# Kernel tuning notes

Hardware: AMD Instinct MI355X
Metric: run time of the kernel (lower is better)

Reference implementation:

```python
import jax, jax.numpy as jnp
import numpy as np

B = 2048          # batch size
L = 8192          # number of fine-grained labels
G = 256           # meta_label_size (number of label groups)
BETA = 0.01       # config.beta


def setup_inputs() -> dict:
    key = jax.random.key(0)
    k1, k2, k3 = jax.random.split(key, 3)
    logits = jax.random.normal(k1, (B, L), dtype=jnp.float32)
    true_y = jax.random.randint(k2, (B, L), 0, 2, dtype=jnp.int32)
    group_ids = jax.random.randint(k3, (L,), 0, G, dtype=jnp.int32)
    return {"logits": logits, "true_y": true_y, "group_ids": group_ids}


def reference(logits, true_y, group_ids):
    # y_hat = sigmoid(logits); meta_prob[b, g] = prod_{l in group g} (1 - y_hat[b, l])
    # Using 1 - sigmoid(x) = sigmoid(-x):
    #   log meta_prob = segment_sum(log_sigmoid(-logits)) over labels per group.
    log_not = jax.nn.log_sigmoid(-logits)                                    # [B, L]
    grp_log = jax.ops.segment_sum(log_not.T, group_ids, num_segments=G).T    # [B, G]
    meta_probs = jnp.exp(grp_log)                                            # [B, G]

    # meta_y[b, g] = 1 if any true label of group g is set in row b (generate_meta_y)
    any_true = jax.ops.segment_sum(true_y.T.astype(jnp.float32), group_ids,
                                   num_segments=G).T                         # [B, G]
    meta_y = (any_true > 0).astype(logits.dtype)

    # BCELoss (mean reduction, torch clamps log terms at -100)
    log_p = jnp.maximum(grp_log, -100.0)
    log_1mp = jnp.maximum(jnp.log1p(-meta_probs), -100.0)
    bce = -jnp.mean(meta_y * log_p + (1.0 - meta_y) * log_1mp)
    return bce * BETA
```

## Files before the change

kernel.cpp:

```cpp
#include <hip/hip_runtime.h>
#include <math.h>

constexpr int   B_    = 2048;
constexpr int   L_    = 8192;
constexpr int   G_    = 256;
constexpr float BETA_ = 0.01f;
constexpr float BIG_  = 1024.0f;

constexpr int   HALF  = L_ / 2;
constexpr int   PMAX  = HALF + G_ * 3;

__device__ __forceinline__ float log_sigmoid_neg(float x) {
    return -(fmaxf(x, 0.0f) + __logf(1.0f + __expf(-fabsf(x))));
}

extern "C" __global__ __launch_bounds__(1024)
void build_rank_kernel(const int* __restrict__ group_ids,
                       int* __restrict__ g_offs,
                       unsigned short* __restrict__ g_rank)
{
    __shared__ int s_cnt[G_];
    __shared__ int s_scan[G_];
    __shared__ int s_cur[G_];

    const int t = threadIdx.x;
    const int h = blockIdx.x;

    if (t < G_) s_cnt[t] = 0;

    const int4 ids = ((const int4*)group_ids)[h * 1024 + t];
    __syncthreads();

    atomicAdd(&s_cnt[ids.x], 1);
    atomicAdd(&s_cnt[ids.y], 1);
    atomicAdd(&s_cnt[ids.z], 1);
    atomicAdd(&s_cnt[ids.w], 1);
    __syncthreads();

    if (t < G_) s_scan[t] = (s_cnt[t] + 3) & ~3;
    __syncthreads();
    for (int off = 1; off < G_; off <<= 1) {
        int v = 0;
        if (t < G_ && t >= off) v = s_scan[t - off];
        __syncthreads();
        if (t < G_) s_scan[t] += v;
        __syncthreads();
    }

    if (t < G_) {
        const int excl = s_scan[t] - ((s_cnt[t] + 3) & ~3);
        s_cur[t] = excl;
        g_offs[h * 257 + t] = excl;
    }
    if (t == 0) g_offs[h * 257 + G_] = s_scan[G_ - 1];
    __syncthreads();

    const int l = h * HALF + t * 4;
    g_rank[l + 0] = (unsigned short)atomicAdd(&s_cur[ids.x], 1);
    g_rank[l + 1] = (unsigned short)atomicAdd(&s_cur[ids.y], 1);
    g_rank[l + 2] = (unsigned short)atomicAdd(&s_cur[ids.z], 1);
    g_rank[l + 3] = (unsigned short)atomicAdd(&s_cur[ids.w], 1);
}


extern "C" __global__ __launch_bounds__(256, 8)
void meta_loss_kernel(const float* __restrict__ logits,
                      const int*   __restrict__ true_y,
                      const int*   __restrict__ g_offs,
                      const unsigned short* __restrict__ g_rank,
                      float*       __restrict__ partial)
{
    __shared__ float s_row[PMAX];

    const int t = threadIdx.x;
    const int b = blockIdx.x >> 1;
    const int h = blockIdx.x & 1;

    const float4*  lg = (const float4*)(logits + (size_t)b * L_ + h * HALF);
    const int4*    ty = (const int4*)(true_y + (size_t)b * L_ + h * HALF);
    const ushort4* rk = (const ushort4*)(g_rank + h * HALF);
    float4* s_row4 = (float4*)s_row;

    const int o0 = g_offs[h * 257 + t];
    const int o1 = g_offs[h * 257 + t + 1];

    #pragma unroll
    for (int i = 0; i < 5; ++i) {
        const int j = i * 256 + t;
        if (j < PMAX / 4) s_row4[j] = make_float4(0.f, 0.f, 0.f, 0.f);
    }
    __syncthreads();

    #pragma unroll
    for (int i = 0; i < HALF / (4 * 256); ++i) {
        const int idx = i * 256 + t;
        const float4  x = lg[idx];
        const int4    y = ty[idx];
        const ushort4 r = rk[idx];
        s_row[r.x] = log_sigmoid_neg(x.x) + (y.x ? BIG_ : 0.0f);
        s_row[r.y] = log_sigmoid_neg(x.y) + (y.y ? BIG_ : 0.0f);
        s_row[r.z] = log_sigmoid_neg(x.z) + (y.z ? BIG_ : 0.0f);
        s_row[r.w] = log_sigmoid_neg(x.w) + (y.w ? BIG_ : 0.0f);
    }
    __syncthreads();

    float4 a4 = make_float4(0.f, 0.f, 0.f, 0.f);
    for (int j = o0; j < o1; j += 4) {
        const float4 v = *(const float4*)&s_row[j];
        a4.x += v.x; a4.y += v.y; a4.z += v.z; a4.w += v.w;
    }
    const float enc = (a4.x + a4.y) + (a4.z + a4.w);

    if (o1 > o0)
        atomicAdd(&partial[b * G_ + t], enc);
}

extern "C" __global__ __launch_bounds__(1024)
void finalize_kernel(const float* __restrict__ partial,
                     float* __restrict__ out)
{
    __shared__ float s_part[16];

    const int t   = threadIdx.x;
    const int idx = blockIdx.x * 1024 + t;

    const float enc = partial[idx];
    const int   k   = __float2int_rn(enc * (1.0f / BIG_));
    const float gl  = enc - BIG_ * (float)k;

    float term;
    if (k != 0) {
        term = fmaxf(gl, -100.0f);
    } else {
        term = fmaxf(log1pf(-__expf(gl)), -100.0f);
    }

    #pragma unroll
    for (int off = 32; off > 0; off >>= 1)
        term += __shfl_down(term, off, 64);
    if ((t & 63) == 0) s_part[t >> 6] = term;
    __syncthreads();

    if (t == 0) {
        float s = 0.0f;
        #pragma unroll
        for (int w = 0; w < 16; ++w) s += s_part[w];
        atomicAdd(out, s * (-BETA_ / ((float)B_ * (float)G_)));
    }
}

extern "C" void kernel_launch(void* const* d_in, const int* in_sizes, int n_in,
                              void* d_out, int out_size, void* d_ws, size_t ws_size,
                              hipStream_t stream) {
    const float* logits    = (const float*)d_in[0];
    const int*   true_y    = (const int*)d_in[1];
    const int*   group_ids = (const int*)d_in[2];
    float*       out       = (float*)d_out;

    float*          partial = (float*)d_ws;
    unsigned short* g_rank  = (unsigned short*)((char*)d_ws + (size_t)B_ * G_ * 4);
    int*            g_offs  = (int*)((char*)d_ws + (size_t)B_ * G_ * 4 + L_ * 2);

    hipMemsetAsync(partial, 0, (size_t)B_ * G_ * 4, stream);
    hipMemsetAsync(out, 0, sizeof(float), stream);

    build_rank_kernel<<<2, 1024, 0, stream>>>(group_ids, g_offs, g_rank);
    meta_loss_kernel<<<2 * B_, 256, 0, stream>>>(logits, true_y, g_offs, g_rank, partial);
    finalize_kernel<<<(B_ * G_) / 1024, 1024, 0, stream>>>(partial, out);
}
```

Measured before the change: 45.28 us.

## Replace scatter-into-sorted-row with permutation gather over 16-label segments

The prep kernel now builds a single global permutation of labels sorted by group, padded to 16-label segments with a sentinel index, plus a per-segment group id. The main kernel uses one 1024-thread block per row: it writes the encoded log-sigmoid values to shared memory in a swizzled order, then each thread gathers one 16-element segment through the permutation and atomically adds the sum to that row's group. This removes the zero-fill and the random shared-memory scatter, at the cost of more atomics per row and indexed shared gathers. It also adds an extra probe kernel that reads half of the logits and throws the result away, which looks like a cache-warming or bandwidth experiment and adds memory traffic.

```diff
diff --git a/kernel.cpp b/kernel.cpp
--- a/kernel.cpp
+++ b/kernel.cpp
@@ -7,37 +7,44 @@
 constexpr float BETA_ = 0.01f;
 constexpr float BIG_  = 1024.0f;
 
-constexpr int   HALF  = L_ / 2;
-constexpr int   PMAX  = HALF + G_ * 3;
+constexpr int   SENTW  = 8192;
+constexpr int   ENCW   = 8256;
+constexpr int   PCAP   = 12032;
+constexpr int   SEGCAP = 768;
 
 __device__ __forceinline__ float log_sigmoid_neg(float x) {
     return -(fmaxf(x, 0.0f) + __logf(1.0f + __expf(-fabsf(x))));
 }
 
+__device__ __forceinline__ int swzF(int l) {
+    return (((l >> 2) & 1) << 12) + ((l >> 3) << 2) + (l & 3);
+}
+
 extern "C" __global__ __launch_bounds__(1024)
-void build_rank_kernel(const int* __restrict__ group_ids,
-                       int* __restrict__ g_offs,
-                       unsigned short* __restrict__ g_rank)
+void prep_kernel(const int* __restrict__ group_ids,
+                 unsigned short* __restrict__ perm,
+                 unsigned char*  __restrict__ seg_gid,
+                 int*            __restrict__ hdr)
 {
     __shared__ int s_cnt[G_];
     __shared__ int s_scan[G_];
     __shared__ int s_cur[G_];
 
     const int t = threadIdx.x;
-    const int h = blockIdx.x;
-
     if (t < G_) s_cnt[t] = 0;
 
-    const int4 ids = ((const int4*)group_ids)[h * 1024 + t];
+    const int4 a = ((const int4*)group_ids)[2 * t];
+    const int4 bq = ((const int4*)group_ids)[2 * t + 1];
     __syncthreads();
 
-    atomicAdd(&s_cnt[ids.x], 1);
-    atomicAdd(&s_cnt[ids.y], 1);
-    atomicAdd(&s_cnt[ids.z], 1);
-    atomicAdd(&s_cnt[ids.w], 1);
+    atomicAdd(&s_cnt[a.x], 1);  atomicAdd(&s_cnt[a.y], 1);
+    atomicAdd(&s_cnt[a.z], 1);  atomicAdd(&s_cnt[a.w], 1);
+    atomicAdd(&s_cnt[bq.x], 1); atomicAdd(&s_cnt[bq.y], 1);
+    atomicAdd(&s_cnt[bq.z], 1); atomicAdd(&s_cnt[bq.w], 1);
     __syncthreads();
 
-    if (t < G_) s_scan[t] = (s_cnt[t] + 3) & ~3;
+    int n = 0, pc = 0;
+    if (t < G_) { n = s_cnt[t]; pc = (n + 15) & ~15; s_scan[t] = pc; }
     __syncthreads();
     for (int off = 1; off < G_; off <<= 1) {
         int v = 0;
@@ -48,71 +55,89 @@
     }
 
     if (t < G_) {
-        const int excl = s_scan[t] - ((s_cnt[t] + 3) & ~3);
-        s_cur[t] = excl;
-        g_offs[h * 257 + t] = excl;
+        const int gbase = s_scan[t] - pc;
+        s_cur[t] = gbase;
+        const int segb = gbase >> 4;
+        for (int i = 0; i < (pc >> 4); ++i) seg_gid[segb + i] = (unsigned char)t;
+        for (int i = n; i < pc; ++i)        perm[gbase + i] = (unsigned short)SENTW;
     }
-    if (t == 0) g_offs[h * 257 + G_] = s_scan[G_ - 1];
+    if (t == 0) hdr[0] = s_scan[G_ - 1] >> 4;
     __syncthreads();
 
-    const int l = h * HALF + t * 4;
-    g_rank[l + 0] = (unsigned short)atomicAdd(&s_cur[ids.x], 1);
-    g_rank[l + 1] = (unsigned short)atomicAdd(&s_cur[ids.y], 1);
-    g_rank[l + 2] = (unsigned short)atomicAdd(&s_cur[ids.z], 1);
-    g_rank[l + 3] = (unsigned short)atomicAdd(&s_cur[ids.w], 1);
+    const int l = 8 * t;
+    perm[atomicAdd(&s_cur[a.x], 1)]  = (unsigned short)swzF(l + 0);
+    perm[atomicAdd(&s_cur[a.y], 1)]  = (unsigned short)swzF(l + 1);
+    perm[atomicAdd(&s_cur[a.z], 1)]  = (unsigned short)swzF(l + 2);
+    perm[atomicAdd(&s_cur[a.w], 1)]  = (unsigned short)swzF(l + 3);
+    perm[atomicAdd(&s_cur[bq.x], 1)] = (unsigned short)swzF(l + 4);
+    perm[atomicAdd(&s_cur[bq.y], 1)] = (unsigned short)swzF(l + 5);
+    perm[atomicAdd(&s_cur[bq.z], 1)] = (unsigned short)swzF(l + 6);
+    perm[atomicAdd(&s_cur[bq.w], 1)] = (unsigned short)swzF(l + 7);
 }
 
+extern "C" __global__ __launch_bounds__(256)
+void probe_kernel(const float* __restrict__ src)
+{
+    const float4* p = (const float4*)src;
+    const size_t  i = (size_t)blockIdx.x * 256 + threadIdx.x;
+    float4 s = make_float4(0.f, 0.f, 0.f, 0.f);
+    #pragma unroll
+    for (int k = 0; k < 4; ++k) {
+        const float4 v = p[i + (size_t)k * 524288];
+        s.x += v.x; s.y += v.y; s.z += v.z; s.w += v.w;
+    }
+    asm volatile("" :: "v"(s.x), "v"(s.y), "v"(s.z), "v"(s.w));
+}
 
-extern "C" __global__ __launch_bounds__(256, 8)
-void meta_loss_kernel(const float* __restrict__ logits,
-                      const int*   __restrict__ true_y,
-                      const int*   __restrict__ g_offs,
-                      const unsigned short* __restrict__ g_rank,
-                      float*       __restrict__ partial)
+extern "C" __global__ __launch_bounds__(1024, 8)
+void meta_gather_kernel(const float* __restrict__ logits,
+                        const int*   __restrict__ true_y,
+                        const unsigned short* __restrict__ perm,
+                        const unsigned char*  __restrict__ seg_gid,
+                        const int*   __restrict__ hdr,
+                        float*       __restrict__ partial)
 {
-    __shared__ float s_row[PMAX];
+    __shared__ float s_enc[ENCW];
 
     const int t = threadIdx.x;
-    const int b = blockIdx.x >> 1;
-    const int h = blockIdx.x & 1;
+    const int b = blockIdx.x;
 
-    const float4*  lg = (const float4*)(logits + (size_t)b * L_ + h * HALF);
-    const int4*    ty = (const int4*)(true_y + (size_t)b * L_ + h * HALF);
-    const ushort4* rk = (const ushort4*)(g_rank + h * HALF);
-    float4* s_row4 = (float4*)s_row;
+    if (t == 0) s_enc[SENTW] = 0.0f;
 
-    const int o0 = g_offs[h * 257 + t];
-    const int o1 = g_offs[h * 257 + t + 1];
+    const float4* lg4 = (const float4*)(logits + (size_t)b * L_);
+    const int4*   ty4 = (const int4*)(true_y + (size_t)b * L_);
 
-    #pragma unroll
-    for (int i = 0; i < 5; ++i) {
-        const int j = i * 256 + t;
-        if (j < PMAX / 4) s_row4[j] = make_float4(0.f, 0.f, 0.f, 0.f);
-    }
+    const float4 x0 = lg4[2 * t];
+    const float4 x1 = lg4[2 * t + 1];
+    const int4   y0 = ty4[2 * t];
+    const int4   y1 = ty4[2 * t + 1];
+
+    float4 E0, E1;
+    E0.x = log_sigmoid_neg(x0.x) + (y0.x ? BIG_ : 0.0f);
+    E0.y = log_sigmoid_neg(x0.y) + (y0.y ? BIG_ : 0.0f);
+    E0.z = log_sigmoid_neg(x0.z) + (y0.z ? BIG_ : 0.0f);
+    E0.w = log_sigmoid_neg(x0.w) + (y0.w ? BIG_ : 0.0f);
+    E1.x = log_sigmoid_neg(x1.x) + (y1.x ? BIG_ : 0.0f);
+    E1.y = log_sigmoid_neg(x1.y) + (y1.y ? BIG_ : 0.0f);
+    E1.z = log_sigmoid_neg(x1.z) + (y1.z ? BIG_ : 0.0f);
+    E1.w = log_sigmoid_neg(x1.w) + (y1.w ? BIG_ : 0.0f);
+
+    ((float4*)s_enc)[t]        = E0;
+    ((float4*)s_enc)[1024 + t] = E1;
     __syncthreads();
 
-    #pragma unroll
-    for (int i = 0; i < HALF / (4 * 256); ++i) {
-        const int idx = i * 256 + t;
-        const float4  x = lg[idx];
-        const int4    y = ty[idx];
-        const ushort4 r = rk[idx];
-        s_row[r.x] = log_sigmoid_neg(x.x) + (y.x ? BIG_ : 0.0f);
-        s_row[r.y] = log_sigmoid_neg(x.y) + (y.y ? BIG_ : 0.0f);
-        s_row[r.z] = log_sigmoid_neg(x.z) + (y.z ? BIG_ : 0.0f);
-        s_row[r.w] = log_sigmoid_neg(x.w) + (y.w ? BIG_ : 0.0f);
+    const int nseg = hdr[0];
+    if (t < nseg) {
+        const int g = seg_gid[t];
+        const ushort4* pp = (const ushort4*)(perm + 16 * t);
+        float s = 0.0f;
+        #pragma unroll
+        for (int k = 0; k < 4; ++k) {
+            const ushort4 q = pp[k];
+            s += s_enc[q.x] + s_enc[q.y] + s_enc[q.z] + s_enc[q.w];
+        }
+        atomicAdd(&partial[(size_t)b * G_ + g], s);
     }
-    __syncthreads();
-
-    float4 a4 = make_float4(0.f, 0.f, 0.f, 0.f);
-    for (int j = o0; j < o1; j += 4) {
-        const float4 v = *(const float4*)&s_row[j];
-        a4.x += v.x; a4.y += v.y; a4.z += v.z; a4.w += v.w;
-    }
-    const float enc = (a4.x + a4.y) + (a4.z + a4.w);
-
-    if (o1 > o0)
-        atomicAdd(&partial[b * G_ + t], enc);
 }
 
 extern "C" __global__ __launch_bounds__(1024)
@@ -144,7 +169,7 @@
     if (t == 0) {
         float s = 0.0f;
         #pragma unroll
-        for (int w = 0; w < 16; ++w) s += s_part[w];
+        for (int wv = 0; wv < 16; ++wv) s += s_part[wv];
         atomicAdd(out, s * (-BETA_ / ((float)B_ * (float)G_)));
     }
 }
@@ -158,13 +183,15 @@
     float*       out       = (float*)d_out;
 
     float*          partial = (float*)d_ws;
-    unsigned short* g_rank  = (unsigned short*)((char*)d_ws + (size_t)B_ * G_ * 4);
-    int*            g_offs  = (int*)((char*)d_ws + (size_t)B_ * G_ * 4 + L_ * 2);
+    unsigned short* perm    = (unsigned short*)((char*)d_ws + 2097152);
+    unsigned char*  seg_gid = (unsigned char*)((char*)d_ws + 2097152 + 24576);
+    int*            hdr     = (int*)((char*)d_ws + 2097152 + 24576 + 1024);
 
     hipMemsetAsync(partial, 0, (size_t)B_ * G_ * 4, stream);
     hipMemsetAsync(out, 0, sizeof(float), stream);
 
-    build_rank_kernel<<<2, 1024, 0, stream>>>(group_ids, g_offs, g_rank);
-    meta_loss_kernel<<<2 * B_, 256, 0, stream>>>(logits, true_y, g_offs, g_rank, partial);
+    prep_kernel<<<1, 1024, 0, stream>>>(group_ids, perm, seg_gid, hdr);
+    probe_kernel<<<2048, 256, 0, stream>>>(logits + (size_t)1024 * L_);
+    meta_gather_kernel<<<B_, 1024, 0, stream>>>(logits, true_y, perm, seg_gid, hdr, partial);
     finalize_kernel<<<(B_ * G_) / 1024, 1024, 0, stream>>>(partial, out);
 }
```

Result: slower. 83.21 us (+83.7%).
